# Kernel tuning notes

Hardware: AMD Instinct MI355X
Metric: run time of the kernel (lower is better)

The kernel has to match this reference:

```python
import jax, jax.numpy as jnp
import numpy as np

L, T, H, F = 16, 2048, 2048, 512  # layers, tokens (B*S=16*128), hidden, features


def setup_inputs() -> dict:
    key = jax.random.key(0)
    k1, k2, k3 = jax.random.split(key, 3)
    x = jax.random.normal(k1, (L, T, H), dtype=jnp.float32)          # stacked residual activations
    W_enc = jax.random.normal(k2, (L, F, H), dtype=jnp.float32) * 0.02  # per-layer encoder (out,in)
    # Dense pack of decoders: W_dec[s, t] is the (source s -> target t) decoder weight (H, F).
    # Only entries with s <= t exist in the original ModuleDict; others are masked to zero in reference().
    W_dec = jax.random.normal(k3, (L, L, H, F), dtype=jnp.float32) * 0.02
    return {"x": x, "W_enc": W_enc, "W_dec": W_dec}


def reference(x, W_enc, W_dec):
    n_layers = x.shape[0]
    # encode: feature_activations[l] = JumpReLU(x[l] @ W_enc[l].T), threshold=0 -> relu
    feats = jax.nn.relu(jnp.einsum('sth,sfh->stf', x, W_enc))  # [L, T, F]
    # causal mask over (source s, target l): decoder exists iff s <= l
    tri = jnp.tril(jnp.ones((n_layers, n_layers), x.dtype))     # tri[l, s] = 1 if s <= l
    Wd = W_dec * tri.T[:, :, None, None]                        # zero out s > l entries
    # reconstruction[l] = sum_{s<=l} feats[s] @ W_dec[s,l].T  (single blocked contraction)
    recon = jnp.einsum('stf,slhf->lth', feats, Wd)              # [L, T, H]
    return feats, recon
```

## Files before the change

### kernel.cpp

```cpp
#include <hip/hip_runtime.h>

#define NL 16
#define NT 2048
#define NH 2048
#define NF 512
#define NPAIR 136

typedef short bf16x8 __attribute__((ext_vector_type(8)));
typedef float f32x4 __attribute__((ext_vector_type(4)));
typedef short s16x4 __attribute__((ext_vector_type(4)));

__device__ __forceinline__ short f2bf(float f) {
  union { float f; unsigned u; } x; x.f = f;
  unsigned r = (x.u + 0x7fffu + ((x.u >> 16) & 1u)) >> 16;
  return (short)r;
}

__device__ __forceinline__ int imin(int a, int b) { return a < b ? a : b; }


__global__ void k_cvt_f32_bf16(const float* __restrict__ src, short* __restrict__ dst, int n4) {
  int i = blockIdx.x * blockDim.x + threadIdx.x;
  const int stride = gridDim.x * blockDim.x;
  for (; i < n4; i += stride) {
    const float4 v = reinterpret_cast<const float4*>(src)[i];
    s16x4 o;
    o[0] = f2bf(v.x); o[1] = f2bf(v.y); o[2] = f2bf(v.z); o[3] = f2bf(v.w);
    reinterpret_cast<s16x4*>(dst)[i] = o;
  }
}

__global__ void k_cvt_wdec(const float* __restrict__ wdec, short* __restrict__ dst) {
  const int p = blockIdx.y;
  int l = 0;
  while ((l + 1) * (l + 2) / 2 <= p) ++l;
  const int s = p - l * (l + 1) / 2;
  const float* src = wdec + (size_t)(s * NL + l) * (NH * NF);
  short* d = dst + (size_t)p * (NH * NF);
  const int n4 = NH * NF / 4;
  for (int i = blockIdx.x * blockDim.x + threadIdx.x; i < n4; i += gridDim.x * blockDim.x) {
    const float4 v = reinterpret_cast<const float4*>(src)[i];
    s16x4 o;
    o[0] = f2bf(v.x); o[1] = f2bf(v.y); o[2] = f2bf(v.z); o[3] = f2bf(v.w);
    reinterpret_cast<s16x4*>(d)[i] = o;
  }
}


__device__ __forceinline__ bf16x8 lds_frag(const short* slot, int r, int cbyte) {
  int byte = (r << 7) + cbyte;
  byte ^= (r & 7) << 4;
  return *reinterpret_cast<const bf16x8*>(reinterpret_cast<const char*>(slot) + byte);
}

__device__ __forceinline__ void stage_half(short* slot, const short* gbase, int ld,
                                           int isA, int h, int tid, int wave) {
#pragma unroll
  for (int j = 0; j < 2; ++j) {
    const int o = j * 8192 + tid * 16;
    const int r = o >> 7;
    const int cb = (o ^ ((r & 7) << 4)) & 127;
    const int g = isA ? (((r >> 6) << 7) + h * 64 + (r & 63))
                      : (((r >> 5) << 6) + h * 32 + (r & 31));
    __builtin_amdgcn_global_load_lds(
        (const __attribute__((address_space(1))) void*)(gbase + (size_t)g * ld + (cb >> 1)),
        (__attribute__((address_space(3))) void*)((char*)slot + j * 8192 + wave * 1024),
        16, 0, 0);
  }
}

template <typename S0, typename S1, typename S2, typename S3>
__device__ __forceinline__ void ktile16(short (*bufc)[8192], f32x4 (&acc)[2][2][4][2],
                                        int wr, int wc, int lane,
                                        S0 s0, S1 s1, S2 s2, S3 s3) {
  const int lr = lane & 15;
  const int ko = (lane >> 4) * 16;
  bf16x8 a0[2][4], a1[2][4], b0[2][2], b1[2][2];
  s0();
#pragma unroll
  for (int kk = 0; kk < 2; ++kk) {
#pragma unroll
    for (int m = 0; m < 4; ++m)
      a0[kk][m] = lds_frag(bufc[0], wr * 64 + m * 16 + lr, kk * 64 + ko);
#pragma unroll
    for (int n = 0; n < 2; ++n)
      b0[kk][n] = lds_frag(bufc[2], wc * 32 + n * 16 + lr, kk * 64 + ko);
  }
  __builtin_amdgcn_s_setprio(1);
#pragma unroll
  for (int kk = 0; kk < 2; ++kk)
#pragma unroll
    for (int m = 0; m < 4; ++m)
#pragma unroll
      for (int n = 0; n < 2; ++n)
        acc[0][0][m][n] = __builtin_amdgcn_mfma_f32_16x16x32_bf16(a0[kk][m], b0[kk][n],
                                                                  acc[0][0][m][n], 0, 0, 0);
  __builtin_amdgcn_s_setprio(0);
  s1();
#pragma unroll
  for (int kk = 0; kk < 2; ++kk)
#pragma unroll
    for (int n = 0; n < 2; ++n)
      b1[kk][n] = lds_frag(bufc[3], wc * 32 + n * 16 + lr, kk * 64 + ko);
  __builtin_amdgcn_s_setprio(1);
#pragma unroll
  for (int kk = 0; kk < 2; ++kk)
#pragma unroll
    for (int m = 0; m < 4; ++m)
#pragma unroll
      for (int n = 0; n < 2; ++n)
        acc[0][1][m][n] = __builtin_amdgcn_mfma_f32_16x16x32_bf16(a0[kk][m], b1[kk][n],
                                                                  acc[0][1][m][n], 0, 0, 0);
  __builtin_amdgcn_s_setprio(0);
  __builtin_amdgcn_s_barrier();
  s2();
#pragma unroll
  for (int kk = 0; kk < 2; ++kk)
#pragma unroll
    for (int m = 0; m < 4; ++m)
      a1[kk][m] = lds_frag(bufc[1], wr * 64 + m * 16 + lr, kk * 64 + ko);
  __builtin_amdgcn_s_setprio(1);
#pragma unroll
  for (int kk = 0; kk < 2; ++kk)
#pragma unroll
    for (int m = 0; m < 4; ++m)
#pragma unroll
      for (int n = 0; n < 2; ++n)
        acc[1][0][m][n] = __builtin_amdgcn_mfma_f32_16x16x32_bf16(a1[kk][m], b0[kk][n],
                                                                  acc[1][0][m][n], 0, 0, 0);
  __builtin_amdgcn_s_setprio(0);
  s3();
  __builtin_amdgcn_s_setprio(1);
#pragma unroll
  for (int kk = 0; kk < 2; ++kk)
#pragma unroll
    for (int m = 0; m < 4; ++m)
#pragma unroll
      for (int n = 0; n < 2; ++n)
        acc[1][1][m][n] = __builtin_amdgcn_mfma_f32_16x16x32_bf16(a1[kk][m], b1[kk][n],
                                                                  acc[1][1][m][n], 0, 0, 0);
  __builtin_amdgcn_s_setprio(0);
  asm volatile("s_waitcnt vmcnt(4)" ::: "memory");
  __builtin_amdgcn_s_barrier();
}


__global__ __launch_bounds__(512, 2) void k_encode256(const short* __restrict__ xbf,
                                                      const short* __restrict__ webf,
                                                      float* __restrict__ feats_f32,
                                                      short* __restrict__ feats_bf) {
  __shared__ short lds[2][4][8192];
  const int l = blockIdx.z;
  const int row0 = blockIdx.y * 256;
  const int col0 = blockIdx.x * 256;
  const int tid = threadIdx.x;
  const int wave = tid >> 6, lane = tid & 63;
  const int wr = wave >> 2, wc = wave & 3;

  const short* A = xbf + (size_t)l * NT * NH + (size_t)row0 * NH;
  const short* B = webf + (size_t)l * NF * NH + (size_t)col0 * NH;

  f32x4 acc[2][2][4][2];
#pragma unroll
  for (int qa = 0; qa < 2; ++qa)
#pragma unroll
    for (int qb = 0; qb < 2; ++qb)
#pragma unroll
      for (int m = 0; m < 4; ++m)
#pragma unroll
        for (int n = 0; n < 2; ++n) {
          f32x4 z = {0.f, 0.f, 0.f, 0.f};
          acc[qa][qb][m][n] = z;
        }

  const int KT = NH / 64;
  stage_half(lds[0][0], A, NH, 1, 0, tid, wave);
  stage_half(lds[0][2], B, NH, 0, 0, tid, wave);
  stage_half(lds[0][1], A, NH, 1, 1, tid, wave);
  stage_half(lds[0][3], B, NH, 0, 1, tid, wave);
  stage_half(lds[1][0], A + 64, NH, 1, 0, tid, wave);
  stage_half(lds[1][2], B + 64, NH, 0, 0, tid, wave);
  asm volatile("s_waitcnt vmcnt(4)" ::: "memory");
  __builtin_amdgcn_s_barrier();

  for (int u = 0; u < KT; ++u) {
    short(*bufc)[8192] = lds[u & 1];
    short(*bufn)[8192] = lds[(u + 1) & 1];
    ktile16(bufc, acc, wr, wc, lane,
            [&] { stage_half(bufn[3], B + imin(u + 1, KT - 1) * 64, NH, 0, 1, tid, wave); },
            [&] { stage_half(bufn[1], A + imin(u + 1, KT - 1) * 64, NH, 1, 1, tid, wave); },
            [&] { stage_half(bufc[2], B + imin(u + 2, KT - 1) * 64, NH, 0, 0, tid, wave); },
            [&] { stage_half(bufc[0], A + imin(u + 2, KT - 1) * 64, NH, 1, 0, tid, wave); });
  }

  const int lr4 = (lane >> 4) * 4, lc = lane & 15;
  float* outF = feats_f32 + (size_t)l * NT * NF;
  short* outB = feats_bf + (size_t)l * NT * NF;
#pragma unroll
  for (int qa = 0; qa < 2; ++qa)
#pragma unroll
    for (int qb = 0; qb < 2; ++qb)
#pragma unroll
      for (int m = 0; m < 4; ++m)
#pragma unroll
        for (int n = 0; n < 2; ++n)
#pragma unroll
          for (int rg = 0; rg < 4; ++rg) {
            const int rr = row0 + wr * 128 + qa * 64 + m * 16 + lr4 + rg;
            const int cc = col0 + wc * 64 + qb * 32 + n * 16 + lc;
            float v = acc[qa][qb][m][n][rg];
            v = v > 0.f ? v : 0.f;
            outF[(size_t)rr * NF + cc] = v;
            outB[(size_t)rr * NF + cc] = f2bf(v);
          }
}


__global__ __launch_bounds__(512, 2) void k_decode256(const short* __restrict__ featsbf,
                                                      const short* __restrict__ wdbf,
                                                      float* __restrict__ recon) {
  __shared__ short lds[2][4][8192];
  const int l = (NL - 1) - blockIdx.z;
  const int row0 = blockIdx.y * 256;
  const int col0 = blockIdx.x * 256;
  const int tid = threadIdx.x;
  const int wave = tid >> 6, lane = tid & 63;
  const int wr = wave >> 2, wc = wave & 3;
  const int pbase = l * (l + 1) / 2;

  const short* Af = featsbf + (size_t)row0 * NF;
  const short* Bw = wdbf + (size_t)col0 * NF;

  f32x4 acc[2][2][4][2];
#pragma unroll
  for (int qa = 0; qa < 2; ++qa)
#pragma unroll
    for (int qb = 0; qb < 2; ++qb)
#pragma unroll
      for (int m = 0; m < 4; ++m)
#pragma unroll
        for (int n = 0; n < 2; ++n) {
          f32x4 z = {0.f, 0.f, 0.f, 0.f};
          acc[qa][qb][m][n] = z;
        }

  const int KT = 8 * (l + 1);
#define ABASE(kt) (Af + (size_t)((kt) >> 3) * (NT * NF) + ((kt)&7) * 64)
#define BBASE(kt) (Bw + (size_t)(pbase + ((kt) >> 3)) * (NH * NF) + ((kt)&7) * 64)

  stage_half(lds[0][0], ABASE(0), NF, 1, 0, tid, wave);
  stage_half(lds[0][2], BBASE(0), NF, 0, 0, tid, wave);
  stage_half(lds[0][1], ABASE(0), NF, 1, 1, tid, wave);
  stage_half(lds[0][3], BBASE(0), NF, 0, 1, tid, wave);
  stage_half(lds[1][0], ABASE(1), NF, 1, 0, tid, wave);
  stage_half(lds[1][2], BBASE(1), NF, 0, 0, tid, wave);
  asm volatile("s_waitcnt vmcnt(4)" ::: "memory");
  __builtin_amdgcn_s_barrier();

  for (int u = 0; u < KT; ++u) {
    short(*bufc)[8192] = lds[u & 1];
    short(*bufn)[8192] = lds[(u + 1) & 1];
    ktile16(bufc, acc, wr, wc, lane,
            [&] { stage_half(bufn[3], BBASE(imin(u + 1, KT - 1)), NF, 0, 1, tid, wave); },
            [&] { stage_half(bufn[1], ABASE(imin(u + 1, KT - 1)), NF, 1, 1, tid, wave); },
            [&] { stage_half(bufc[2], BBASE(imin(u + 2, KT - 1)), NF, 0, 0, tid, wave); },
            [&] { stage_half(bufc[0], ABASE(imin(u + 2, KT - 1)), NF, 1, 0, tid, wave); });
  }
#undef ABASE
#undef BBASE

  const int lr4 = (lane >> 4) * 4, lc = lane & 15;
  float* out = recon + (size_t)l * NT * NH;
#pragma unroll
  for (int qa = 0; qa < 2; ++qa)
#pragma unroll
    for (int qb = 0; qb < 2; ++qb)
#pragma unroll
      for (int m = 0; m < 4; ++m)
#pragma unroll
        for (int n = 0; n < 2; ++n)
#pragma unroll
          for (int rg = 0; rg < 4; ++rg) {
            const int rr = row0 + wr * 128 + qa * 64 + m * 16 + lr4 + rg;
            const int cc = col0 + wc * 64 + qb * 32 + n * 16 + lc;
            out[(size_t)rr * NH + cc] = acc[qa][qb][m][n][rg];
          }
}


extern "C" void kernel_launch(void* const* d_in, const int* in_sizes, int n_in,
                              void* d_out, int out_size, void* d_ws, size_t ws_size,
                              hipStream_t stream) {
  const float* x = (const float*)d_in[0];
  const float* wenc = (const float*)d_in[1];
  const float* wdec = (const float*)d_in[2];

  float* feats_f32 = (float*)d_out;
  float* recon = feats_f32 + (size_t)NL * NT * NF;

  short* x_bf = (short*)d_ws;
  short* we_bf = x_bf + (size_t)NL * NT * NH;
  short* wd_bf = we_bf + (size_t)NL * NF * NH;
  short* ft_bf = wd_bf + (size_t)NPAIR * NH * NF;

  k_cvt_f32_bf16<<<2048, 256, 0, stream>>>(x, x_bf, NL * NT * NH / 4);
  k_cvt_f32_bf16<<<2048, 256, 0, stream>>>(wenc, we_bf, NL * NF * NH / 4);
  k_cvt_wdec<<<dim3(512, NPAIR), 256, 0, stream>>>(wdec, wd_bf);

  k_encode256<<<dim3(2, 8, 16), 512, 0, stream>>>(x_bf, we_bf, feats_f32, ft_bf);
  k_decode256<<<dim3(8, 8, 16), 512, 0, stream>>>(ft_bf, wd_bf, recon);
}
```

Measured before the change: 837.6 us.

## Replace interleaved 8-wave half-tile pipeline with simple double-buffered full-tile prefetch

Replaces the staggered half-tile staging schedule with a plain double buffer. It previously issued four partial loads interleaved between MFMA phases and kept two tiles in flight with a mid-tile barrier. Now the whole next k-tile is issued at the start of each iteration, all fragments are loaded up front, the MFMA groups are merged, and it waits on vmcnt(0) with one barrier per tile. This simplifies the schedule and removes the extra barrier and the clamped redundant loads. In exchange, prefetch depth drops to one tile and the full drain each iteration can expose global load latency.

```diff
diff --git a/kernel.cpp b/kernel.cpp
--- a/kernel.cpp
+++ b/kernel.cpp
@@ -69,22 +69,32 @@
   }
 }
 
-template <typename S0, typename S1, typename S2, typename S3>
-__device__ __forceinline__ void ktile16(short (*bufc)[8192], f32x4 (&acc)[2][2][4][2],
-                                        int wr, int wc, int lane,
-                                        S0 s0, S1 s1, S2 s2, S3 s3) {
+__device__ __forceinline__ void stage_tile(short (*buf)[8192], const short* At,
+                                           const short* Bt, int lda, int ldb,
+                                           int tid, int wave) {
+  stage_half(buf[0], At, lda, 1, 0, tid, wave);
+  stage_half(buf[1], At, lda, 1, 1, tid, wave);
+  stage_half(buf[2], Bt, ldb, 0, 0, tid, wave);
+  stage_half(buf[3], Bt, ldb, 0, 1, tid, wave);
+}
+
+template <typename SFn>
+__device__ __forceinline__ void ktile_flat(short (*bufc)[8192], f32x4 (&acc)[2][2][4][2],
+                                           int wr, int wc, int lane, SFn stagefn) {
   const int lr = lane & 15;
   const int ko = (lane >> 4) * 16;
-  bf16x8 a0[2][4], a1[2][4], b0[2][2], b1[2][2];
-  s0();
+  stagefn();
+  bf16x8 b0[2][2], b1[2][2], a0[2][4], a1[2][4];
 #pragma unroll
   for (int kk = 0; kk < 2; ++kk) {
 #pragma unroll
+    for (int n = 0; n < 2; ++n) {
+      b0[kk][n] = lds_frag(bufc[2], wc * 32 + n * 16 + lr, kk * 64 + ko);
+      b1[kk][n] = lds_frag(bufc[3], wc * 32 + n * 16 + lr, kk * 64 + ko);
+    }
+#pragma unroll
     for (int m = 0; m < 4; ++m)
       a0[kk][m] = lds_frag(bufc[0], wr * 64 + m * 16 + lr, kk * 64 + ko);
-#pragma unroll
-    for (int n = 0; n < 2; ++n)
-      b0[kk][n] = lds_frag(bufc[2], wc * 32 + n * 16 + lr, kk * 64 + ko);
   }
   __builtin_amdgcn_s_setprio(1);
 #pragma unroll
@@ -92,28 +102,13 @@
 #pragma unroll
     for (int m = 0; m < 4; ++m)
 #pragma unroll
-      for (int n = 0; n < 2; ++n)
+      for (int n = 0; n < 2; ++n) {
         acc[0][0][m][n] = __builtin_amdgcn_mfma_f32_16x16x32_bf16(a0[kk][m], b0[kk][n],
                                                                   acc[0][0][m][n], 0, 0, 0);
-  __builtin_amdgcn_s_setprio(0);
-  s1();
-#pragma unroll
-  for (int kk = 0; kk < 2; ++kk)
-#pragma unroll
-    for (int n = 0; n < 2; ++n)
-      b1[kk][n] = lds_frag(bufc[3], wc * 32 + n * 16 + lr, kk * 64 + ko);
-  __builtin_amdgcn_s_setprio(1);
-#pragma unroll
-  for (int kk = 0; kk < 2; ++kk)
-#pragma unroll
-    for (int m = 0; m < 4; ++m)
-#pragma unroll
-      for (int n = 0; n < 2; ++n)
         acc[0][1][m][n] = __builtin_amdgcn_mfma_f32_16x16x32_bf16(a0[kk][m], b1[kk][n],
                                                                   acc[0][1][m][n], 0, 0, 0);
+      }
   __builtin_amdgcn_s_setprio(0);
-  __builtin_amdgcn_s_barrier();
-  s2();
 #pragma unroll
   for (int kk = 0; kk < 2; ++kk)
 #pragma unroll
@@ -125,22 +120,14 @@
 #pragma unroll
     for (int m = 0; m < 4; ++m)
 #pragma unroll
-      for (int n = 0; n < 2; ++n)
+      for (int n = 0; n < 2; ++n) {
         acc[1][0][m][n] = __builtin_amdgcn_mfma_f32_16x16x32_bf16(a1[kk][m], b0[kk][n],
                                                                   acc[1][0][m][n], 0, 0, 0);
-  __builtin_amdgcn_s_setprio(0);
-  s3();
-  __builtin_amdgcn_s_setprio(1);
-#pragma unroll
-  for (int kk = 0; kk < 2; ++kk)
-#pragma unroll
-    for (int m = 0; m < 4; ++m)
-#pragma unroll
-      for (int n = 0; n < 2; ++n)
         acc[1][1][m][n] = __builtin_amdgcn_mfma_f32_16x16x32_bf16(a1[kk][m], b1[kk][n],
                                                                   acc[1][1][m][n], 0, 0, 0);
+      }
   __builtin_amdgcn_s_setprio(0);
-  asm volatile("s_waitcnt vmcnt(4)" ::: "memory");
+  asm volatile("s_waitcnt vmcnt(0) lgkmcnt(0)" ::: "memory");
   __builtin_amdgcn_s_barrier();
 }
 
@@ -174,23 +161,17 @@
         }
 
   const int KT = NH / 64;
-  stage_half(lds[0][0], A, NH, 1, 0, tid, wave);
-  stage_half(lds[0][2], B, NH, 0, 0, tid, wave);
-  stage_half(lds[0][1], A, NH, 1, 1, tid, wave);
-  stage_half(lds[0][3], B, NH, 0, 1, tid, wave);
-  stage_half(lds[1][0], A + 64, NH, 1, 0, tid, wave);
-  stage_half(lds[1][2], B + 64, NH, 0, 0, tid, wave);
-  asm volatile("s_waitcnt vmcnt(4)" ::: "memory");
+  stage_tile(lds[0], A, B, NH, NH, tid, wave);
+  asm volatile("s_waitcnt vmcnt(0)" ::: "memory");
   __builtin_amdgcn_s_barrier();
 
   for (int u = 0; u < KT; ++u) {
     short(*bufc)[8192] = lds[u & 1];
     short(*bufn)[8192] = lds[(u + 1) & 1];
-    ktile16(bufc, acc, wr, wc, lane,
-            [&] { stage_half(bufn[3], B + imin(u + 1, KT - 1) * 64, NH, 0, 1, tid, wave); },
-            [&] { stage_half(bufn[1], A + imin(u + 1, KT - 1) * 64, NH, 1, 1, tid, wave); },
-            [&] { stage_half(bufc[2], B + imin(u + 2, KT - 1) * 64, NH, 0, 0, tid, wave); },
-            [&] { stage_half(bufc[0], A + imin(u + 2, KT - 1) * 64, NH, 1, 0, tid, wave); });
+    ktile_flat(bufc, acc, wr, wc, lane, [&] {
+      if (u + 1 < KT)
+        stage_tile(bufn, A + (u + 1) * 64, B + (u + 1) * 64, NH, NH, tid, wave);
+    });
   }
 
   const int lr4 = (lane >> 4) * 4, lc = lane & 15;
@@ -248,23 +229,17 @@
 #define ABASE(kt) (Af + (size_t)((kt) >> 3) * (NT * NF) + ((kt)&7) * 64)
 #define BBASE(kt) (Bw + (size_t)(pbase + ((kt) >> 3)) * (NH * NF) + ((kt)&7) * 64)
 
-  stage_half(lds[0][0], ABASE(0), NF, 1, 0, tid, wave);
-  stage_half(lds[0][2], BBASE(0), NF, 0, 0, tid, wave);
-  stage_half(lds[0][1], ABASE(0), NF, 1, 1, tid, wave);
-  stage_half(lds[0][3], BBASE(0), NF, 0, 1, tid, wave);
-  stage_half(lds[1][0], ABASE(1), NF, 1, 0, tid, wave);
-  stage_half(lds[1][2], BBASE(1), NF, 0, 0, tid, wave);
-  asm volatile("s_waitcnt vmcnt(4)" ::: "memory");
+  stage_tile(lds[0], ABASE(0), BBASE(0), NF, NF, tid, wave);
+  asm volatile("s_waitcnt vmcnt(0)" ::: "memory");
   __builtin_amdgcn_s_barrier();
 
   for (int u = 0; u < KT; ++u) {
     short(*bufc)[8192] = lds[u & 1];
     short(*bufn)[8192] = lds[(u + 1) & 1];
-    ktile16(bufc, acc, wr, wc, lane,
-            [&] { stage_half(bufn[3], BBASE(imin(u + 1, KT - 1)), NF, 0, 1, tid, wave); },
-            [&] { stage_half(bufn[1], ABASE(imin(u + 1, KT - 1)), NF, 1, 1, tid, wave); },
-            [&] { stage_half(bufc[2], BBASE(imin(u + 2, KT - 1)), NF, 0, 0, tid, wave); },
-            [&] { stage_half(bufc[0], ABASE(imin(u + 2, KT - 1)), NF, 1, 0, tid, wave); });
+    ktile_flat(bufc, acc, wr, wc, lane, [&] {
+      if (u + 1 < KT)
+        stage_tile(bufn, ABASE(u + 1), BBASE(u + 1), NF, NF, tid, wave);
+    });
   }
 #undef ABASE
 #undef BBASE
```

Result: faster. 821.1 us (-2.0%).
